# Optimization experiments

Measured on AMD Instinct MI355X. Metric: run time of the kernel, lower is better.

## Reference

```python
import jax, jax.numpy as jnp
import numpy as np

DIAG = 4  # number of distinct power-of-2 diagonal bands; must divide H


def _diag_mask(H, L):
    # head h in group g = h // (H // DIAG) uses tril diagonal offset 2**g - 1.
    # True entries are MASKED (filled with -inf), except the last key column
    # which is always kept (cur_mask[:, -1] = 0 in the torch code).
    group = H // DIAG
    offs = 2 ** (jnp.arange(H) // group) - 1            # [H]
    rows = jnp.arange(L)[:, None]                        # [L,1] query index
    cols = jnp.arange(L)[None, :]                        # [1,L] key index
    mask = (cols <= rows + offs[:, None, None]) & (cols != L - 1)  # [H,L,L]
    return mask


def setup_inputs() -> dict:
    key = jax.random.key(0)
    kq, kk, kv = jax.random.split(key, 3)
    B, L, H, E = 4, 2048, 16, 64
    queries = jax.random.normal(kq, (B, L, H, E), dtype=jnp.float32)
    keys = jax.random.normal(kk, (B, L, H, E), dtype=jnp.float32)
    values = jax.random.normal(kv, (B, L, H, E), dtype=jnp.float32)
    return {"queries": queries, "keys": keys, "values": values}


def reference(queries, keys, values):
    B, L, H, E = queries.shape
    scale = 1.0 / np.sqrt(E).astype(np.float32)
    # [B,H,L,S]
    scores = jnp.einsum('blhe,bshe->bhls', queries, keys)
    mask = _diag_mask(H, L)                              # [H,L,L]
    scores = jnp.where(mask[None], -jnp.inf, scores)
    A = jax.nn.softmax(scale * scores, axis=-1)          # dropout inactive (eval)
    V = jnp.einsum('bhls,bshd->blhd', A, values)
    return V
```

## Files before the change

### kernel.cpp

```cpp
#include <hip/hip_runtime.h>
#include <stdint.h>

using f32x4  = __attribute__((ext_vector_type(4))) float;
using f32x16 = __attribute__((ext_vector_type(16))) float;
using s16x8  = __attribute__((ext_vector_type(8))) short;
using u16x4  = __attribute__((ext_vector_type(4))) unsigned short;
using u32x4  = __attribute__((ext_vector_type(4))) unsigned int;

typedef __attribute__((address_space(3))) unsigned int lds_u32;
typedef __attribute__((address_space(1))) unsigned int glb_u32;

__device__ __forceinline__ unsigned short f2bf(float f){
  union { float f; unsigned u; } x; x.f = f;
  return (unsigned short)((x.u + 0x7FFFu + ((x.u >> 16) & 1u)) >> 16);
}
__device__ __forceinline__ unsigned cvt_pk(float lo, float hi){
  unsigned r;
  asm("v_cvt_pk_bf16_f32 %0, %1, %2" : "=v"(r) : "v"(lo), "v"(hi));
  return r;
}
__device__ __forceinline__ void plswap(unsigned &a, unsigned &b){
  asm volatile("v_permlane32_swap_b32 %0, %1" : "+v"(a), "+v"(b));
}

#if __has_builtin(__builtin_amdgcn_exp2f)
#define EXP2F(x) __builtin_amdgcn_exp2f(x)
#else
#define EXP2F(x) exp2f(x)
#endif

#define MFMA16(A,B,C) __builtin_amdgcn_mfma_f32_16x16x32_bf16((A),(B),(C),0,0,0)
#define MFMA32(A,B,C) __builtin_amdgcn_mfma_f32_32x32x16_bf16((A),(B),(C),0,0,0)

constexpr int   L      = 2048;
constexpr int   H      = 16;
constexpr int   E      = 64;
constexpr int   HE     = 1024;
constexpr float SCALE  = 0.125f;
constexpr float QSCALE = 0.18033688011112042f;

__global__ __launch_bounds__(256)
void prep_kv(const float* __restrict__ Kg, const float* __restrict__ Vg,
             unsigned short* __restrict__ Ko, unsigned short* __restrict__ Vo){
  __shared__ __align__(16) unsigned short t8[4096];
  const int g0 = blockIdx.x;
  const int t  = threadIdx.x;
  if (g0 < 2048){
    const int gid = g0;
    const int jt = gid & 31, bh = gid >> 5;
    const int b = bh >> 4, h = bh & 15;
    const int key6 = t >> 2;
    const int p    = t & 3;
    const int kb = key6 >> 5, k31 = key6 & 31;
    const float* src = Kg + ((size_t)((b*2048 + jt*64 + key6)*16 + h) << 6) + p*16;
    const float4 v0 = *reinterpret_cast<const float4*>(src);
    const float4 v1 = *reinterpret_cast<const float4*>(src + 4);
    const float4 v2 = *reinterpret_cast<const float4*>(src + 8);
    const float4 v3 = *reinterpret_cast<const float4*>(src + 12);
    s16x8 f0, f1;
    f0[0]=(short)f2bf(v0.x); f0[1]=(short)f2bf(v0.y); f0[2]=(short)f2bf(v0.z); f0[3]=(short)f2bf(v0.w);
    f0[4]=(short)f2bf(v1.x); f0[5]=(short)f2bf(v1.y); f0[6]=(short)f2bf(v1.z); f0[7]=(short)f2bf(v1.w);
    f1[0]=(short)f2bf(v2.x); f1[1]=(short)f2bf(v2.y); f1[2]=(short)f2bf(v2.z); f1[3]=(short)f2bf(v2.w);
    f1[4]=(short)f2bf(v3.x); f1[5]=(short)f2bf(v3.y); f1[6]=(short)f2bf(v3.z); f1[7]=(short)f2bf(v3.w);
    const int slot0 = ((kb*4 + p)*2 + 0)*32 + k31;
    *reinterpret_cast<s16x8*>(&t8[slot0*8])      = f0;
    *reinterpret_cast<s16x8*>(&t8[(slot0+32)*8]) = f1;
    __syncthreads();
    unsigned short* dst = Ko + ((size_t)gid << 12) + t*16;
    *reinterpret_cast<s16x8*>(dst)     = *reinterpret_cast<const s16x8*>(&t8[t*16]);
    *reinterpret_cast<s16x8*>(dst + 8) = *reinterpret_cast<const s16x8*>(&t8[t*16 + 8]);
  } else {
    const int gid = g0 - 2048;
    const int jt = gid & 31, bh = gid >> 5;
    const int b = bh >> 4, h = bh & 15;
    const int key6 = t >> 2;
    const int p    = t & 3;
    const int kc = key6 >> 4, h2 = (key6 >> 3) & 1, kr = key6 & 7;
    const float* src = Vg + ((size_t)((b*2048 + jt*64 + key6)*16 + h) << 6) + p*16;
    float vv[16];
    #pragma unroll
    for (int q = 0; q < 4; ++q){
      const float4 v = *reinterpret_cast<const float4*>(src + q*4);
      vv[q*4+0]=v.x; vv[q*4+1]=v.y; vv[q*4+2]=v.z; vv[q*4+3]=v.w;
    }
    #pragma unroll
    for (int j = 0; j < 16; ++j){
      const int e  = p*16 + j;
      const int eb = e >> 5, e31 = e & 31;
      const int slot = ((eb*4 + kc)*2 + h2)*32 + e31;
      t8[slot*8 + kr] = f2bf(vv[j]);
    }
    __syncthreads();
    unsigned short* dst = Vo + ((size_t)gid << 12) + t*16;
    *reinterpret_cast<s16x8*>(dst)     = *reinterpret_cast<const s16x8*>(&t8[t*16]);
    *reinterpret_cast<s16x8*>(dst + 8) = *reinterpret_cast<const s16x8*>(&t8[t*16 + 8]);
  }
}

__global__ __launch_bounds__(128, 4)
void attn12(const float* __restrict__ Qg, const unsigned short* __restrict__ Kbg,
            const unsigned short* __restrict__ Vtg, float* __restrict__ Og)
{
  __shared__ __align__(16) unsigned short Kbuf[2][4096];
  __shared__ __align__(16) unsigned short Vbuf[2][4096];

  const int tid  = threadIdx.x;
  const int wave = tid >> 6;
  const int lane = tid & 63;
  const int c    = lane & 31;
  const int hi   = lane >> 5;

  const int gid = blockIdx.x;
  const int qc  = gid >> 6;
  const int bh  = gid & 63;
  const int b = bh >> 4, h = bh & 15;
  const int off = (1 << (h >> 2)) - 1;

  const int    qrow0 = 64 * qc + wave * 32;
  const size_t fbase = (size_t)b * L * HE + (size_t)h * 64;
  const size_t tbase = (size_t)bh * 32;

  s16x8 qf[4];
  {
    const float* qp_ = Qg + fbase + (size_t)(qrow0 + c) * HE;
    #pragma unroll
    for (int ec = 0; ec < 4; ++ec){
      const float4 a  = *reinterpret_cast<const float4*>(qp_ + ec*16 + hi*8);
      const float4 b2 = *reinterpret_cast<const float4*>(qp_ + ec*16 + hi*8 + 4);
      s16x8 v;
      v[0]=(short)f2bf(a.x*QSCALE);  v[1]=(short)f2bf(a.y*QSCALE);
      v[2]=(short)f2bf(a.z*QSCALE);  v[3]=(short)f2bf(a.w*QSCALE);
      v[4]=(short)f2bf(b2.x*QSCALE); v[5]=(short)f2bf(b2.y*QSCALE);
      v[6]=(short)f2bf(b2.z*QSCALE); v[7]=(short)f2bf(b2.w*QSCALE);
      qf[ec] = v;
    }
  }

  s16x8 ones;
  #pragma unroll
  for (int j = 0; j < 8; ++j) ones[j] = (short)0x3F80;

  f32x16 acc0, acc1, accl;
  #pragma unroll
  for (int r = 0; r < 16; ++r){ acc0[r]=0.f; acc1[r]=0.f; accl[r]=0.f; }

  const int j0   = qc;
  const int qlim = qrow0 + c + off;

  auto STAGE = [&](int jt, int nb){
    const unsigned short* gk = Kbg + ((size_t)(tbase + jt) << 12) + (size_t)(wave*2048 + lane*8);
    const unsigned short* gv = Vtg + ((size_t)(tbase + jt) << 12) + (size_t)(wave*2048 + lane*8);
    #pragma unroll
    for (int i = 0; i < 4; ++i)
      __builtin_amdgcn_global_load_lds((const glb_u32*)(gk + i*512),
          (lds_u32*)&Kbuf[nb][wave*2048 + i*512], 16, 0, 0);
    #pragma unroll
    for (int i = 0; i < 4; ++i)
      __builtin_amdgcn_global_load_lds((const glb_u32*)(gv + i*512),
          (lds_u32*)&Vbuf[nb][wave*2048 + i*512], 16, 0, 0);
  };

  auto COMP = [&](int jt, int nb){
    const int s0 = jt * 64;
    const unsigned short* KB = Kbuf[nb];
    const unsigned short* VB = Vbuf[nb];

    f32x16 S0, S1;
    #pragma unroll
    for (int r = 0; r < 16; ++r){ S0[r]=0.f; S1[r]=0.f; }
    __builtin_amdgcn_s_setprio(1);
    #pragma unroll
    for (int ec = 0; ec < 4; ++ec){
      const s16x8 k0 = *reinterpret_cast<const s16x8*>(&KB[(((0*4+ec)*2+hi)*32 + c)*8]);
      const s16x8 k1 = *reinterpret_cast<const s16x8*>(&KB[(((1*4+ec)*2+hi)*32 + c)*8]);
      S0 = MFMA32(k0, qf[ec], S0);
      S1 = MFMA32(k1, qf[ec], S1);
    }
    __builtin_amdgcn_s_setprio(0);

    if ((jt == 31) || (s0 <= qrow0 + 31 + off)){
      #pragma unroll
      for (int r = 0; r < 16; ++r){
        const int kg0 = s0 + (r&3) + 8*(r>>2) + 4*hi;
        const int kg1 = kg0 + 32;
        if (!((kg0 > qlim) || (kg0 == L-1))) S0[r] = -1e30f;
        if (!((kg1 > qlim) || (kg1 == L-1))) S1[r] = -1e30f;
      }
    }

    #pragma unroll
    for (int r = 0; r < 16; ++r){
      S0[r] = EXP2F(S0[r]);
      S1[r] = EXP2F(S1[r]);
    }

    __builtin_amdgcn_s_setprio(1);
    #define PV_STEP(Pv, kh, kcg) { \
      unsigned a0 = cvt_pk(Pv[8*(kh)+0], Pv[8*(kh)+1]); \
      unsigned a1 = cvt_pk(Pv[8*(kh)+2], Pv[8*(kh)+3]); \
      unsigned b0 = cvt_pk(Pv[8*(kh)+4], Pv[8*(kh)+5]); \
      unsigned b1 = cvt_pk(Pv[8*(kh)+6], Pv[8*(kh)+7]); \
      plswap(a0, b0); plswap(a1, b1); \
      u32x4 afu; afu[0]=a0; afu[1]=a1; afu[2]=b0; afu[3]=b1; \
      const s16x8 af = __builtin_bit_cast(s16x8, afu); \
      const s16x8 vf0 = *reinterpret_cast<const s16x8*>(&VB[(((0*4+(kcg))*2+hi)*32 + c)*8]); \
      const s16x8 vf1 = *reinterpret_cast<const s16x8*>(&VB[(((1*4+(kcg))*2+hi)*32 + c)*8]); \
      acc0 = MFMA32(af, vf0, acc0); \
      acc1 = MFMA32(af, vf1, acc1); \
      accl = MFMA32(af, ones, accl); \
    }
    PV_STEP(S0, 0, 0)
    PV_STEP(S0, 1, 1)
    PV_STEP(S1, 0, 2)
    PV_STEP(S1, 1, 3)
    #undef PV_STEP
    __builtin_amdgcn_s_setprio(0);
  };

  #define WAITBAR8 asm volatile("s_waitcnt vmcnt(8)\n\ts_barrier" ::: "memory")
  #define WAITBAR0 asm volatile("s_waitcnt vmcnt(0)\n\ts_barrier" ::: "memory")
  #define BARRIER  __builtin_amdgcn_s_barrier()

  STAGE(j0, j0 & 1);
  {
    const int j1 = (j0 + 1 <= 31) ? (j0 + 1) : 31;
    STAGE(j1, (j0 + 1) & 1);
  }

  for (int jt = j0; jt < 30; ++jt){
    WAITBAR8;
    COMP(jt, jt & 1);
    BARRIER;
    STAGE(jt + 2, jt & 1);
  }
  WAITBAR8;
  COMP(30, 0);
  WAITBAR0;
  COMP(31, 1);

  #undef WAITBAR8
  #undef WAITBAR0
  #undef BARRIER

  #pragma unroll
  for (int r = 0; r < 16; ++r){
    const int rowr = (r&3) + 8*(r>>2) + 4*hi;
    const float li = 1.0f / accl[r];
    float* op = Og + fbase + (size_t)(qrow0 + rowr) * HE;
    op[c]      = acc0[r] * li;
    op[32 + c] = acc1[r] * li;
  }
}

__global__ __launch_bounds__(512)
void attn_band(const float* __restrict__ Qg, const float* __restrict__ Kg,
               const float* __restrict__ Vg, float* __restrict__ Og)
{
  __shared__ __align__(16) unsigned short Ks[64*64];
  __shared__ __align__(16) unsigned short Vs[64*64];
  __shared__ __align__(16) unsigned short Ps[8][16*64];
  const int tid  = threadIdx.x;
  const int wave = tid >> 6;
  const int lane = tid & 63;
  const int lo16 = lane & 15;
  const int hi4  = lane >> 4;
  const int gid = blockIdx.x;
  const int qb  = gid & 15;
  const int bh  = gid >> 4;
  const int b   = bh >> 4;
  const int h   = bh & 15;
  const int off = (1 << (h >> 2)) - 1;
  const int    r0   = qb * 128;
  const size_t base = (size_t)b * L * HE + (size_t)h * 64;
  const int qrow0 = r0 + wave * 16;
  s16x8 qf[2];
  {
    const float* qp = Qg + base + (size_t)(qrow0 + lo16) * HE;
    #pragma unroll
    for (int ec = 0; ec < 2; ++ec){
      const int e0 = ec*32 + hi4*8;
      s16x8 v;
      #pragma unroll
      for (int j = 0; j < 8; ++j) v[j] = (short)f2bf(qp[e0 + j]);
      qf[ec] = v;
    }
  }
  f32x4 acc[4];
  #pragma unroll
  for (int et = 0; et < 4; ++et) acc[et] = f32x4{0.f,0.f,0.f,0.f};
  float m_run[4], l_run[4];
  #pragma unroll
  for (int i = 0; i < 4; ++i){ m_run[i] = -1e30f; l_run[i] = 0.f; }
  const int j0 = (r0 + off + 1) >> 6;
  for (int jt = j0; jt < 32; ++jt){
    const int s0 = jt * 64;
    __syncthreads();
    {
      const int f4    = tid & 15;
      const int rbase = tid >> 4;
      #pragma unroll
      for (int p = 0; p < 2; ++p){
        const int row = p*32 + rbase;
        const float4 vv = *reinterpret_cast<const float4*>(
            Kg + base + (size_t)(s0 + row) * HE + f4*4);
        u16x4 w; w[0]=f2bf(vv.x); w[1]=f2bf(vv.y); w[2]=f2bf(vv.z); w[3]=f2bf(vv.w);
        const int idx = row*64 + ((f4*4) ^ ((row & 7) << 3));
        *reinterpret_cast<u16x4*>(&Ks[idx]) = w;
      }
    }
    {
      const int kb = tid >> 5;
      const int e0 = (tid & 31) * 2;
      float2 cc[4];
      #pragma unroll
      for (int j = 0; j < 4; ++j)
        cc[j] = *reinterpret_cast<const float2*>(
            Vg + base + (size_t)(s0 + 4*kb + j) * HE + e0);
      #pragma unroll
      for (int i = 0; i < 2; ++i){
        const int e = e0 + i;
        u16x4 w;
        w[0] = f2bf(i ? cc[0].y : cc[0].x);
        w[1] = f2bf(i ? cc[1].y : cc[1].x);
        w[2] = f2bf(i ? cc[2].y : cc[2].x);
        w[3] = f2bf(i ? cc[3].y : cc[3].x);
        const int idx = e*64 + ((kb*4) ^ ((e & 7) << 3));
        *reinterpret_cast<u16x4*>(&Vs[idx]) = w;
      }
    }
    __syncthreads();
    if (jt < 31 && s0 + 63 <= qrow0 + off) continue;
    f32x4 S[4];
    #pragma unroll
    for (int kt = 0; kt < 4; ++kt){
      const int key = kt*16 + lo16;
      f32x4 z = {0.f,0.f,0.f,0.f};
      #pragma unroll
      for (int ec = 0; ec < 2; ++ec){
        const int e = ec*32 + hi4*8;
        const s16x8 kf = *reinterpret_cast<const s16x8*>(
            &Ks[key*64 + (e ^ ((key & 7) << 3))]);
        z = MFMA16(qf[ec], kf, z);
      }
      S[kt] = z;
    }
    #pragma unroll
    for (int kt = 0; kt < 4; ++kt){
      const int kg = s0 + kt*16 + lo16;
      #pragma unroll
      for (int i = 0; i < 4; ++i){
        const int qg2 = qrow0 + hi4*4 + i;
        const bool ok = (kg > qg2 + off) || (kg == L-1);
        S[kt][i] = ok ? S[kt][i]*SCALE : -1e30f;
      }
    }
    #pragma unroll
    for (int i = 0; i < 4; ++i){
      float t = fmaxf(fmaxf(S[0][i],S[1][i]), fmaxf(S[2][i],S[3][i]));
      t = fmaxf(t, __shfl_xor(t,1));
      t = fmaxf(t, __shfl_xor(t,2));
      t = fmaxf(t, __shfl_xor(t,4));
      t = fmaxf(t, __shfl_xor(t,8));
      const float mn = fmaxf(m_run[i], t);
      const float rs = __expf(m_run[i] - mn);
      m_run[i]  = mn;
      l_run[i] *= rs;
      acc[0][i] *= rs; acc[1][i] *= rs; acc[2][i] *= rs; acc[3][i] *= rs;
    }
    unsigned short* pwv = Ps[wave];
    float rsum[4] = {0.f,0.f,0.f,0.f};
    #pragma unroll
    for (int kt = 0; kt < 4; ++kt){
      #pragma unroll
      for (int i = 0; i < 4; ++i){
        const float p = __expf(S[kt][i] - m_run[i]);
        rsum[i] += p;
        const int qr  = hi4*4 + i;
        const int col = kt*16 + lo16;
        pwv[qr*64 + (col ^ ((qr & 7) << 3))] = f2bf(p);
      }
    }
    #pragma unroll
    for (int i = 0; i < 4; ++i){
      float t = rsum[i];
      t += __shfl_xor(t,1); t += __shfl_xor(t,2);
      t += __shfl_xor(t,4); t += __shfl_xor(t,8);
      l_run[i] += t;
    }
    #pragma unroll
    for (int kc = 0; kc < 2; ++kc){
      const int kk = kc*32 + hi4*8;
      const s16x8 pf = *reinterpret_cast<const s16x8*>(
          &pwv[lo16*64 + (kk ^ ((lo16 & 7) << 3))]);
      #pragma unroll
      for (int et = 0; et < 4; ++et){
        const int e = et*16 + lo16;
        const s16x8 vf = *reinterpret_cast<const s16x8*>(
            &Vs[e*64 + (kk ^ ((e & 7) << 3))]);
        acc[et] = MFMA16(pf, vf, acc[et]);
      }
    }
  }
  #pragma unroll
  for (int i = 0; i < 4; ++i){
    const float inv = 1.0f / l_run[i];
    const int   qg2 = qrow0 + hi4*4 + i;
    float* op = Og + base + (size_t)qg2 * HE;
    #pragma unroll
    for (int et = 0; et < 4; ++et)
      op[et*16 + lo16] = acc[et][i] * inv;
  }
}

extern "C" void kernel_launch(void* const* d_in, const int* in_sizes, int n_in,
                              void* d_out, int out_size, void* d_ws, size_t ws_size,
                              hipStream_t stream) {
  const float* Q = (const float*)d_in[0];
  const float* K = (const float*)d_in[1];
  const float* V = (const float*)d_in[2];
  float* O = (float*)d_out;

  const size_t kb_bytes = (size_t)64 * 32 * 4096 * 2;
  const size_t need     = kb_bytes * 2;
  if (ws_size >= need) {
    unsigned short* Kb = (unsigned short*)d_ws;
    unsigned short* Vt = (unsigned short*)((char*)d_ws + kb_bytes);
    prep_kv<<<dim3(4096), dim3(256), 0, stream>>>(K, V, Kb, Vt);
    attn12 <<<dim3(2048), dim3(128), 0, stream>>>(Q, Kb, Vt, O);
  } else {
    attn_band<<<dim3(1024), dim3(512), 0, stream>>>(Q, K, V, O);
  }
}
```

Before: 84.74 us.

## Use 8-wave blocks of 256 query rows sharing K/V tiles with balanced ordering

Each block now has 8 waves covering 256 query rows instead of 2 waves covering 64, so every staged K/V tile in LDS is reused by four times as many waves and global/LDS staging traffic per query drops. Block order pairs early and late query chunks (qb = u or 11-u) to balance the causal-band workload, and waves whose rows are fully masked for a tile skip the compute. The trade-offs are fewer blocks (512) with less occupancy flexibility, and barriers that make the fastest waves wait for the slowest in the larger group.

```diff
diff --git a/kernel.cpp b/kernel.cpp
--- a/kernel.cpp
+++ b/kernel.cpp
@@ -97,8 +97,8 @@
   }
 }
 
-__global__ __launch_bounds__(128, 4)
-void attn12(const float* __restrict__ Qg, const unsigned short* __restrict__ Kbg,
+__global__ __launch_bounds__(512, 4)
+void attn13(const float* __restrict__ Qg, const unsigned short* __restrict__ Kbg,
             const unsigned short* __restrict__ Vtg, float* __restrict__ Og)
 {
   __shared__ __align__(16) unsigned short Kbuf[2][4096];
@@ -111,12 +111,13 @@
   const int hi   = lane >> 5;
 
   const int gid = blockIdx.x;
-  const int qc  = gid >> 6;
+  const int u   = gid >> 6;
   const int bh  = gid & 63;
+  const int qb  = (u < 4) ? u : (11 - u);
   const int b = bh >> 4, h = bh & 15;
   const int off = (1 << (h >> 2)) - 1;
 
-  const int    qrow0 = 64 * qc + wave * 32;
+  const int    qrow0 = 256 * qb + wave * 32;
   const size_t fbase = (size_t)b * L * HE + (size_t)h * 64;
   const size_t tbase = (size_t)bh * 32;
 
@@ -144,24 +145,21 @@
   #pragma unroll
   for (int r = 0; r < 16; ++r){ acc0[r]=0.f; acc1[r]=0.f; accl[r]=0.f; }
 
-  const int j0   = qc;
+  const int j0   = 4 * qb;
   const int qlim = qrow0 + c + off;
 
   auto STAGE = [&](int jt, int nb){
-    const unsigned short* gk = Kbg + ((size_t)(tbase + jt) << 12) + (size_t)(wave*2048 + lane*8);
-    const unsigned short* gv = Vtg + ((size_t)(tbase + jt) << 12) + (size_t)(wave*2048 + lane*8);
-    #pragma unroll
-    for (int i = 0; i < 4; ++i)
-      __builtin_amdgcn_global_load_lds((const glb_u32*)(gk + i*512),
-          (lds_u32*)&Kbuf[nb][wave*2048 + i*512], 16, 0, 0);
-    #pragma unroll
-    for (int i = 0; i < 4; ++i)
-      __builtin_amdgcn_global_load_lds((const glb_u32*)(gv + i*512),
-          (lds_u32*)&Vbuf[nb][wave*2048 + i*512], 16, 0, 0);
+    const unsigned short* gk = Kbg + ((size_t)(tbase + jt) << 12) + (size_t)(wave*512 + lane*8);
+    const unsigned short* gv = Vtg + ((size_t)(tbase + jt) << 12) + (size_t)(wave*512 + lane*8);
+    __builtin_amdgcn_global_load_lds((const glb_u32*)gk,
+        (lds_u32*)&Kbuf[nb][wave*512], 16, 0, 0);
+    __builtin_amdgcn_global_load_lds((const glb_u32*)gv,
+        (lds_u32*)&Vbuf[nb][wave*512], 16, 0, 0);
   };
 
   auto COMP = [&](int jt, int nb){
     const int s0 = jt * 64;
+    if ((jt < 31) && (s0 + 63 <= qrow0 + off)) return;
     const unsigned short* KB = Kbuf[nb];
     const unsigned short* VB = Vbuf[nb];
 
@@ -217,28 +215,25 @@
     __builtin_amdgcn_s_setprio(0);
   };
 
-  #define WAITBAR8 asm volatile("s_waitcnt vmcnt(8)\n\ts_barrier" ::: "memory")
+  #define WAITBAR2 asm volatile("s_waitcnt vmcnt(2)\n\ts_barrier" ::: "memory")
   #define WAITBAR0 asm volatile("s_waitcnt vmcnt(0)\n\ts_barrier" ::: "memory")
   #define BARRIER  __builtin_amdgcn_s_barrier()
 
-  STAGE(j0, j0 & 1);
-  {
-    const int j1 = (j0 + 1 <= 31) ? (j0 + 1) : 31;
-    STAGE(j1, (j0 + 1) & 1);
-  }
+  STAGE(j0, 0);
+  STAGE(j0 + 1, 1);
 
   for (int jt = j0; jt < 30; ++jt){
-    WAITBAR8;
+    WAITBAR2;
     COMP(jt, jt & 1);
     BARRIER;
     STAGE(jt + 2, jt & 1);
   }
-  WAITBAR8;
+  WAITBAR2;
   COMP(30, 0);
   WAITBAR0;
   COMP(31, 1);
 
-  #undef WAITBAR8
+  #undef WAITBAR2
   #undef WAITBAR0
   #undef BARRIER
 
@@ -426,7 +421,7 @@
     unsigned short* Kb = (unsigned short*)d_ws;
     unsigned short* Vt = (unsigned short*)((char*)d_ws + kb_bytes);
     prep_kv<<<dim3(4096), dim3(256), 0, stream>>>(K, V, Kb, Vt);
-    attn12 <<<dim3(2048), dim3(128), 0, stream>>>(Q, Kb, Vt, O);
+    attn13 <<<dim3(512),  dim3(512), 0, stream>>>(Q, Kb, Vt, O);
   } else {
     attn_band<<<dim3(1024), dim3(512), 0, stream>>>(Q, K, V, O);
   }
```

New measurement: 72.03 us. -15.0%, faster.
